# Kernel tuning notes

Measured on AMD Instinct MI355X. Metric: run time of the kernel, lower is better.

## Reference

```python
import jax, jax.numpy as jnp
import numpy as np

N_NODES = 50000
N_EDGES = 800000
D_IN = 64
D_OUT = 64


def setup_inputs() -> dict:
    key = jax.random.key(0)
    k1, k2, k3 = jax.random.split(key, 3)
    x = jax.random.normal(k1, (N_NODES, D_IN), dtype=jnp.float32)
    edge_index = jax.random.randint(k2, (2, N_EDGES), 0, N_NODES, dtype=jnp.int64)
    W = jax.random.normal(k3, (D_IN, D_OUT), dtype=jnp.float32) / np.sqrt(D_IN)
    b = jnp.zeros((D_OUT,), dtype=jnp.float32)
    return {"x": x, "edge_index": edge_index, "W": W, "b": b}


def reference(x, edge_index, W, b):
    # GCNConv with default add_self_loops=True and symmetric normalization,
    # followed by ReLU (GCN_layer activation).
    N = x.shape[0]
    loop = jnp.arange(N, dtype=edge_index.dtype)
    row = jnp.concatenate([edge_index[0], loop])  # source nodes [E+N]
    col = jnp.concatenate([edge_index[1], loop])  # target nodes [E+N]

    # degree of target nodes (includes self-loops)
    deg = jax.ops.segment_sum(jnp.ones_like(col, dtype=x.dtype), col, num_segments=N)
    deg_inv_sqrt = jnp.where(deg > 0, jax.lax.rsqrt(jnp.maximum(deg, 1.0)), 0.0)
    norm = deg_inv_sqrt[row] * deg_inv_sqrt[col]  # [E+N]

    xw = x @ W  # [N, Dout] - linear before propagation (as in PyG GCNConv)
    msg = norm[:, None] * xw[row]  # gather + per-edge scale, [E+N, Dout]
    out = jax.ops.segment_sum(msg, col, num_segments=N) + b  # scatter-add
    return jax.nn.relu(out)
```

## Files before the change

kernel.cpp:

```cpp
#include <hip/hip_runtime.h>

#define N_NODES 50000
#define N_EDGES 800000
#define D 64
#define CAP 64
#define NBLK_MM (N_NODES / 16)
#define NBLK_DEG (N_EDGES / 256)

typedef _Float16 half4_t __attribute__((ext_vector_type(4)));
typedef _Float16 half8_t __attribute__((ext_vector_type(8)));

__device__ __forceinline__ unsigned debase(unsigned v) {
    return (v >= 0x80000000u) ? v - 0xAAAAAAAAu : v;
}

__global__ __launch_bounds__(256) void k_mm_degbucket(const float* __restrict__ x,
                                                      const float* __restrict__ W,
                                                      _Float16* __restrict__ xwh,
                                                      const int* __restrict__ ei,
                                                      unsigned* __restrict__ deg,
                                                      unsigned short* __restrict__ ebuf) {
    __shared__ float Wl[D * D];
    __shared__ float xl[16 * D];
    int bid = blockIdx.x >> 1;
    if (blockIdx.x & 1) {
        int e = bid * 256 + threadIdx.x;
        int r = ei[e];
        int c = ei[N_EDGES + e];
        unsigned k = debase(atomicAdd(&deg[c], 1u));
        ebuf[(c << 6) | k] = (unsigned short)r;
        return;
    }
    int tid = threadIdx.x;
#pragma unroll
    for (int i = tid; i < D * D / 4; i += 256)
        ((float4*)Wl)[i] = ((const float4*)W)[i];
    int r0 = bid * 16;
    ((float4*)xl)[tid] = ((const float4*)(x + (size_t)r0 * D))[tid];
    __syncthreads();
    int c4 = tid & 15;
    int rs = tid >> 4;
    const float* xrow = &xl[rs * D];
    const float* wc   = &Wl[c4 * 4];
    float acc0 = 0.f, acc1 = 0.f, acc2 = 0.f, acc3 = 0.f;
#pragma unroll
    for (int k4 = 0; k4 < 16; ++k4) {
        float4 xv = *(const float4*)(xrow + k4 * 4);
        float4 w0 = *(const float4*)(wc + (k4 * 4 + 0) * D);
        float4 w1 = *(const float4*)(wc + (k4 * 4 + 1) * D);
        float4 w2 = *(const float4*)(wc + (k4 * 4 + 2) * D);
        float4 w3 = *(const float4*)(wc + (k4 * 4 + 3) * D);
        acc0 = fmaf(xv.x, w0.x, fmaf(xv.y, w1.x, fmaf(xv.z, w2.x, fmaf(xv.w, w3.x, acc0))));
        acc1 = fmaf(xv.x, w0.y, fmaf(xv.y, w1.y, fmaf(xv.z, w2.y, fmaf(xv.w, w3.y, acc1))));
        acc2 = fmaf(xv.x, w0.z, fmaf(xv.y, w1.z, fmaf(xv.z, w2.z, fmaf(xv.w, w3.z, acc2))));
        acc3 = fmaf(xv.x, w0.w, fmaf(xv.y, w1.w, fmaf(xv.z, w2.w, fmaf(xv.w, w3.w, acc3))));
    }
    half4_t h = { (_Float16)acc0, (_Float16)acc1, (_Float16)acc2, (_Float16)acc3 };
    *(half4_t*)(xwh + (size_t)(r0 + rs) * D + c4 * 4) = h;
}

#define GSTEP(JLIT)                                                            \
    {                                                                          \
        int   rj = __builtin_amdgcn_ds_swizzle(sl, ((JLIT) << 5) | 24);        \
        float sj = __int_as_float(                                             \
            __builtin_amdgcn_ds_swizzle(__float_as_int(s), ((JLIT) << 5) | 24)); \
        half8_t v = *(const half8_t*)(xwh + (size_t)rj * D + c8 * 8);          \
        _Pragma("unroll")                                                      \
        for (int i = 0; i < 8; ++i) acc[i] = fmaf(sj, (float)v[i], acc[i]);    \
    }

__global__ __launch_bounds__(256) void k_gather8(const unsigned* __restrict__ deg,
                                                 const unsigned short* __restrict__ ebuf,
                                                 const _Float16* __restrict__ xwh,
                                                 const float* __restrict__ b,
                                                 float* __restrict__ out) {
    int wid = blockIdx.x * 4 + (threadIdx.x >> 6);
    if (wid >= N_NODES / 8) return;
    int lane = threadIdx.x & 63;
    int G    = lane >> 3;
    int c8   = lane & 7;
    int node = wid * 8 + G;
    int cnt  = (int)debase(deg[node]);
    int m = cnt;
    m = max(m, __shfl_xor(m, 8, 64));
    m = max(m, __shfl_xor(m, 16, 64));
    m = max(m, __shfl_xor(m, 32, 64));
    int rounds = (m + 7) >> 3;
    const unsigned short* eb = ebuf + ((size_t)node << 6);
    int   sl = (int)eb[c8];
    float dv = (float)debase(deg[sl]);
    float acc[8] = {0.f,0.f,0.f,0.f,0.f,0.f,0.f,0.f};
    for (int R = 0; R < rounds; ++R) {
        int rb   = R << 3;
        int rb_n = (rb + 8 < CAP) ? rb + 8 : rb;
        int   sl_n = (int)eb[rb_n + c8];
        float dv_n = (float)debase(deg[sl_n]);
        float s = (rb + c8 < cnt) ? rsqrtf(dv + 1.0f) : 0.0f;
        GSTEP(0) GSTEP(1) GSTEP(2) GSTEP(3)
        GSTEP(4) GSTEP(5) GSTEP(6) GSTEP(7)
        sl = sl_n; dv = dv_n;
    }
    float dc = rsqrtf((float)(cnt + 1));
    half8_t xv = *(const half8_t*)(xwh + (size_t)node * D + c8 * 8);
    float4 b0 = *(const float4*)(b + c8 * 8);
    float4 b1 = *(const float4*)(b + c8 * 8 + 4);
    float o[8];
#pragma unroll
    for (int i = 0; i < 8; ++i)
        o[i] = dc * fmaf(dc, (float)xv[i], acc[i]);
    o[0] += b0.x; o[1] += b0.y; o[2] += b0.z; o[3] += b0.w;
    o[4] += b1.x; o[5] += b1.y; o[6] += b1.z; o[7] += b1.w;
#pragma unroll
    for (int i = 0; i < 8; ++i) o[i] = o[i] > 0.f ? o[i] : 0.f;
    float4 v0 = {o[0], o[1], o[2], o[3]};
    float4 v1 = {o[4], o[5], o[6], o[7]};
    *(float4*)(out + (size_t)node * D + c8 * 8)     = v0;
    *(float4*)(out + (size_t)node * D + c8 * 8 + 4) = v1;
}

extern "C" void kernel_launch(void* const* d_in, const int* in_sizes, int n_in,
                              void* d_out, int out_size, void* d_ws, size_t ws_size,
                              hipStream_t stream) {
    const float* x  = (const float*)d_in[0];
    const int*   ei = (const int*)d_in[1];
    const float* W  = (const float*)d_in[2];
    const float* b  = (const float*)d_in[3];
    float* out = (float*)d_out;

    char* ws = (char*)d_ws;
    size_t off = 0;
    _Float16*       xwh  = (_Float16*)(ws + off);       off += (size_t)N_NODES * D * sizeof(_Float16);
    unsigned*       deg  = (unsigned*)(ws + off);       off += (size_t)N_NODES * sizeof(unsigned);
    unsigned short* ebuf = (unsigned short*)(ws + off); off += (size_t)N_NODES * CAP * sizeof(unsigned short);

    k_mm_degbucket<<<NBLK_MM + NBLK_DEG, 256, 0, stream>>>(x, W, xwh, ei, deg, ebuf);
    k_gather8<<<(N_NODES / 8 + 3) / 4, 256, 0, stream>>>(deg, ebuf, xwh, b, out);
}
```

Measured before the change: 124.5 us.

## Cache byte-packed degree table in LDS with persistent gather blocks

The gather kernel now runs 256 persistent blocks of 1024 threads. Each block first loads the whole degree array into shared memory, packed as one byte per node, and then loops over chunks of 128 nodes. Neighbour degree lookups become LDS reads instead of scattered global loads, which removes the prefetch of the next neighbour's degree. In exchange every block reads all 200 KB of degree data up front and uses 50 KB of LDS, which limits occupancy. Packing to one byte assumes degrees stay below 256; the 64-slot bucket cap already makes that true.

```diff
diff --git a/kernel.cpp b/kernel.cpp
--- a/kernel.cpp
+++ b/kernel.cpp
@@ -6,6 +6,7 @@
 #define CAP 64
 #define NBLK_MM (N_NODES / 16)
 #define NBLK_DEG (N_EDGES / 256)
+#define NCHUNK ((N_NODES + 127) / 128)
 
 typedef _Float16 half4_t __attribute__((ext_vector_type(4)));
 typedef _Float16 half8_t __attribute__((ext_vector_type(8)));
@@ -69,53 +70,65 @@
         for (int i = 0; i < 8; ++i) acc[i] = fmaf(sj, (float)v[i], acc[i]);    \
     }
 
-__global__ __launch_bounds__(256) void k_gather8(const unsigned* __restrict__ deg,
-                                                 const unsigned short* __restrict__ ebuf,
-                                                 const _Float16* __restrict__ xwh,
-                                                 const float* __restrict__ b,
-                                                 float* __restrict__ out) {
-    int wid = blockIdx.x * 4 + (threadIdx.x >> 6);
-    if (wid >= N_NODES / 8) return;
-    int lane = threadIdx.x & 63;
+__global__ __launch_bounds__(1024) void k_gather_lds(const unsigned* __restrict__ deg,
+                                                     const unsigned short* __restrict__ ebuf,
+                                                     const _Float16* __restrict__ xwh,
+                                                     const float* __restrict__ b,
+                                                     float* __restrict__ out) {
+    __shared__ unsigned char dl[N_NODES];
+    int tid = threadIdx.x;
+    for (int i = tid; i < N_NODES / 4; i += 1024) {
+        const unsigned* dp = deg + i * 4;
+        unsigned p = (debase(dp[0]) & 0xffu)
+                   | ((debase(dp[1]) & 0xffu) << 8)
+                   | ((debase(dp[2]) & 0xffu) << 16)
+                   | ((debase(dp[3]) & 0xffu) << 24);
+        ((unsigned*)dl)[i] = p;
+    }
+    __syncthreads();
+    int wv   = tid >> 6;
+    int lane = tid & 63;
     int G    = lane >> 3;
     int c8   = lane & 7;
-    int node = wid * 8 + G;
-    int cnt  = (int)debase(deg[node]);
-    int m = cnt;
-    m = max(m, __shfl_xor(m, 8, 64));
-    m = max(m, __shfl_xor(m, 16, 64));
-    m = max(m, __shfl_xor(m, 32, 64));
-    int rounds = (m + 7) >> 3;
-    const unsigned short* eb = ebuf + ((size_t)node << 6);
-    int   sl = (int)eb[c8];
-    float dv = (float)debase(deg[sl]);
-    float acc[8] = {0.f,0.f,0.f,0.f,0.f,0.f,0.f,0.f};
-    for (int R = 0; R < rounds; ++R) {
-        int rb   = R << 3;
-        int rb_n = (rb + 8 < CAP) ? rb + 8 : rb;
-        int   sl_n = (int)eb[rb_n + c8];
-        float dv_n = (float)debase(deg[sl_n]);
-        float s = (rb + c8 < cnt) ? rsqrtf(dv + 1.0f) : 0.0f;
-        GSTEP(0) GSTEP(1) GSTEP(2) GSTEP(3)
-        GSTEP(4) GSTEP(5) GSTEP(6) GSTEP(7)
-        sl = sl_n; dv = dv_n;
+    for (int chunk = blockIdx.x; chunk < NCHUNK; chunk += 256) {
+        int nbase = chunk * 128 + wv * 8;
+        if (nbase >= N_NODES) continue;
+        int node = nbase + G;
+        int cnt  = (int)dl[node];
+        int m = cnt;
+        m = max(m, __shfl_xor(m, 8, 64));
+        m = max(m, __shfl_xor(m, 16, 64));
+        m = max(m, __shfl_xor(m, 32, 64));
+        int rounds = (m + 7) >> 3;
+        const unsigned short* eb = ebuf + ((size_t)node << 6);
+        int sl = (int)eb[c8];
+        float acc[8] = {0.f,0.f,0.f,0.f,0.f,0.f,0.f,0.f};
+        for (int R = 0; R < rounds; ++R) {
+            int rb   = R << 3;
+            int rb_n = (rb + 8 < CAP) ? rb + 8 : rb;
+            int sl_n = (int)eb[rb_n + c8];
+            float s = (rb + c8 < cnt) ? rsqrtf((float)dl[sl] + 1.0f) : 0.0f;
+            GSTEP(0) GSTEP(1) GSTEP(2) GSTEP(3)
+            GSTEP(4) GSTEP(5) GSTEP(6) GSTEP(7)
+            sl = sl_n;
+        }
+        float dc = rsqrtf((float)(cnt + 1));
+        half8_t xv = *(const half8_t*)(xwh + (size_t)node * D + c8 * 8);
+        float4 b0 = *(const float4*)(b + c8 * 8);
+        float4 b1 = *(const float4*)(b + c8 * 8 + 4);
+        float o[8];
+#pragma unroll
+        for (int i = 0; i < 8; ++i)
+            o[i] = dc * fmaf(dc, (float)xv[i], acc[i]);
+        o[0] += b0.x; o[1] += b0.y; o[2] += b0.z; o[3] += b0.w;
+        o[4] += b1.x; o[5] += b1.y; o[6] += b1.z; o[7] += b1.w;
+#pragma unroll
+        for (int i = 0; i < 8; ++i) o[i] = o[i] > 0.f ? o[i] : 0.f;
+        float4 v0 = {o[0], o[1], o[2], o[3]};
+        float4 v1 = {o[4], o[5], o[6], o[7]};
+        *(float4*)(out + (size_t)node * D + c8 * 8)     = v0;
+        *(float4*)(out + (size_t)node * D + c8 * 8 + 4) = v1;
     }
-    float dc = rsqrtf((float)(cnt + 1));
-    half8_t xv = *(const half8_t*)(xwh + (size_t)node * D + c8 * 8);
-    float4 b0 = *(const float4*)(b + c8 * 8);
-    float4 b1 = *(const float4*)(b + c8 * 8 + 4);
-    float o[8];
-#pragma unroll
-    for (int i = 0; i < 8; ++i)
-        o[i] = dc * fmaf(dc, (float)xv[i], acc[i]);
-    o[0] += b0.x; o[1] += b0.y; o[2] += b0.z; o[3] += b0.w;
-    o[4] += b1.x; o[5] += b1.y; o[6] += b1.z; o[7] += b1.w;
-#pragma unroll
-    for (int i = 0; i < 8; ++i) o[i] = o[i] > 0.f ? o[i] : 0.f;
-    float4 v0 = {o[0], o[1], o[2], o[3]};
-    float4 v1 = {o[4], o[5], o[6], o[7]};
-    *(float4*)(out + (size_t)node * D + c8 * 8)     = v0;
-    *(float4*)(out + (size_t)node * D + c8 * 8 + 4) = v1;
 }
 
 extern "C" void kernel_launch(void* const* d_in, const int* in_sizes, int n_in,
@@ -134,5 +147,5 @@
     unsigned short* ebuf = (unsigned short*)(ws + off); off += (size_t)N_NODES * CAP * sizeof(unsigned short);
 
     k_mm_degbucket<<<NBLK_MM + NBLK_DEG, 256, 0, stream>>>(x, W, xwh, ei, deg, ebuf);
-    k_gather8<<<(N_NODES / 8 + 3) / 4, 256, 0, stream>>>(deg, ebuf, xwh, b, out);
+    k_gather_lds<<<256, 1024, 0, stream>>>(deg, ebuf, xwh, b, out);
 }
```

Result: slower. 128.8 us (+3.5%).

## Split gather into two column-half passes with 16 nodes per wavefront

Applied to the files above, without the earlier changes.

The gather kernel now packs 16 destination nodes per wavefront, with 4 lanes per node covering 32 of the 64 feature columns. It is launched twice, once per column half, so each pass reads only half of every xwh row. The aim is a smaller gather working set per pass for better cache hit rates, and less padding waste from rounding edge counts up to 4 instead of 8. The cost is reading the edge bucket and degrees twice, running the max-degree loop twice, and an extra kernel launch.

```diff
diff --git a/kernel.cpp b/kernel.cpp
--- a/kernel.cpp
+++ b/kernel.cpp
@@ -6,6 +6,7 @@
 #define CAP 64
 #define NBLK_MM (N_NODES / 16)
 #define NBLK_DEG (N_EDGES / 256)
+#define NW16 (N_NODES / 16)
 
 typedef _Float16 half4_t __attribute__((ext_vector_type(4)));
 typedef _Float16 half8_t __attribute__((ext_vector_type(8)));
@@ -59,51 +60,52 @@
     *(half4_t*)(xwh + (size_t)(r0 + rs) * D + c4 * 4) = h;
 }
 
-#define GSTEP(JLIT)                                                            \
+#define HSTEP(JLIT)                                                            \
     {                                                                          \
-        int   rj = __builtin_amdgcn_ds_swizzle(sl, ((JLIT) << 5) | 24);        \
+        int   rj = __builtin_amdgcn_ds_swizzle(sl, ((JLIT) << 5) | 28);        \
         float sj = __int_as_float(                                             \
-            __builtin_amdgcn_ds_swizzle(__float_as_int(s), ((JLIT) << 5) | 24)); \
-        half8_t v = *(const half8_t*)(xwh + (size_t)rj * D + c8 * 8);          \
+            __builtin_amdgcn_ds_swizzle(__float_as_int(s), ((JLIT) << 5) | 28)); \
+        half8_t v = *(const half8_t*)(xwh + (size_t)rj * D + C0 + q * 8);      \
         _Pragma("unroll")                                                      \
         for (int i = 0; i < 8; ++i) acc[i] = fmaf(sj, (float)v[i], acc[i]);    \
     }
 
-__global__ __launch_bounds__(256) void k_gather8(const unsigned* __restrict__ deg,
-                                                 const unsigned short* __restrict__ ebuf,
-                                                 const _Float16* __restrict__ xwh,
-                                                 const float* __restrict__ b,
-                                                 float* __restrict__ out) {
+__global__ __launch_bounds__(256) void k_gather16(const unsigned* __restrict__ deg,
+                                                  const unsigned short* __restrict__ ebuf,
+                                                  const _Float16* __restrict__ xwh,
+                                                  const float* __restrict__ b,
+                                                  float* __restrict__ out,
+                                                  int C0) {
     int wid = blockIdx.x * 4 + (threadIdx.x >> 6);
-    if (wid >= N_NODES / 8) return;
+    if (wid >= NW16) return;
     int lane = threadIdx.x & 63;
-    int G    = lane >> 3;
-    int c8   = lane & 7;
-    int node = wid * 8 + G;
+    int G    = lane >> 2;
+    int q    = lane & 3;
+    int node = wid * 16 + G;
     int cnt  = (int)debase(deg[node]);
     int m = cnt;
+    m = max(m, __shfl_xor(m, 4, 64));
     m = max(m, __shfl_xor(m, 8, 64));
     m = max(m, __shfl_xor(m, 16, 64));
     m = max(m, __shfl_xor(m, 32, 64));
-    int rounds = (m + 7) >> 3;
+    int rounds = (m + 3) >> 2;
     const unsigned short* eb = ebuf + ((size_t)node << 6);
-    int   sl = (int)eb[c8];
+    int   sl = (int)eb[q];
     float dv = (float)debase(deg[sl]);
     float acc[8] = {0.f,0.f,0.f,0.f,0.f,0.f,0.f,0.f};
     for (int R = 0; R < rounds; ++R) {
-        int rb   = R << 3;
-        int rb_n = (rb + 8 < CAP) ? rb + 8 : rb;
-        int   sl_n = (int)eb[rb_n + c8];
+        int rb   = R << 2;
+        int rb_n = (rb + 4 < CAP) ? rb + 4 : rb;
+        int   sl_n = (int)eb[rb_n + q];
         float dv_n = (float)debase(deg[sl_n]);
-        float s = (rb + c8 < cnt) ? rsqrtf(dv + 1.0f) : 0.0f;
-        GSTEP(0) GSTEP(1) GSTEP(2) GSTEP(3)
-        GSTEP(4) GSTEP(5) GSTEP(6) GSTEP(7)
+        float s = (rb + q < cnt) ? rsqrtf(dv + 1.0f) : 0.0f;
+        HSTEP(0) HSTEP(1) HSTEP(2) HSTEP(3)
         sl = sl_n; dv = dv_n;
     }
     float dc = rsqrtf((float)(cnt + 1));
-    half8_t xv = *(const half8_t*)(xwh + (size_t)node * D + c8 * 8);
-    float4 b0 = *(const float4*)(b + c8 * 8);
-    float4 b1 = *(const float4*)(b + c8 * 8 + 4);
+    half8_t xv = *(const half8_t*)(xwh + (size_t)node * D + C0 + q * 8);
+    float4 b0 = *(const float4*)(b + C0 + q * 8);
+    float4 b1 = *(const float4*)(b + C0 + q * 8 + 4);
     float o[8];
 #pragma unroll
     for (int i = 0; i < 8; ++i)
@@ -114,8 +116,8 @@
     for (int i = 0; i < 8; ++i) o[i] = o[i] > 0.f ? o[i] : 0.f;
     float4 v0 = {o[0], o[1], o[2], o[3]};
     float4 v1 = {o[4], o[5], o[6], o[7]};
-    *(float4*)(out + (size_t)node * D + c8 * 8)     = v0;
-    *(float4*)(out + (size_t)node * D + c8 * 8 + 4) = v1;
+    *(float4*)(out + (size_t)node * D + C0 + q * 8)     = v0;
+    *(float4*)(out + (size_t)node * D + C0 + q * 8 + 4) = v1;
 }
 
 extern "C" void kernel_launch(void* const* d_in, const int* in_sizes, int n_in,
@@ -134,5 +136,6 @@
     unsigned short* ebuf = (unsigned short*)(ws + off); off += (size_t)N_NODES * CAP * sizeof(unsigned short);
 
     k_mm_degbucket<<<NBLK_MM + NBLK_DEG, 256, 0, stream>>>(x, W, xwh, ei, deg, ebuf);
-    k_gather8<<<(N_NODES / 8 + 3) / 4, 256, 0, stream>>>(deg, ebuf, xwh, b, out);
+    k_gather16<<<(NW16 + 3) / 4, 256, 0, stream>>>(deg, ebuf, xwh, b, out, 0);
+    k_gather16<<<(NW16 + 3) / 4, 256, 0, stream>>>(deg, ebuf, xwh, b, out, 32);
 }
```

Result: slower. 142.6 us (+14.6%).
